# Kernel tuning notes

Hardware: AMD Instinct MI355X
Metric: run time of the kernel (lower is better)

## Reference

```python
import jax, jax.numpy as jnp
import numpy as np

D_MODEL, D_STATE, D_CONV, EXPAND, DT_RANK = 2048, 16, 4, 2, 128
D_INNER = EXPAND * D_MODEL
BATCH, SEQLEN = 4, 2048


def setup_inputs() -> dict:
    key = jax.random.key(0)
    ks = jax.random.split(key, 10)
    s = lambda fan_in: 1.0 / np.sqrt(fan_in)
    hidden_states = jax.random.normal(ks[0], (BATCH, SEQLEN, D_MODEL), jnp.float32)
    W_in = jax.random.normal(ks[1], (2 * D_INNER, D_MODEL), jnp.float32) * s(D_MODEL)
    conv_w = jax.random.normal(ks[2], (D_INNER, D_CONV), jnp.float32) * s(D_CONV)
    conv_b = jax.random.normal(ks[3], (D_INNER,), jnp.float32) * 0.02
    W_x = jax.random.normal(ks[4], (DT_RANK + 2 * D_STATE, D_INNER), jnp.float32) * s(D_INNER)
    W_dt = jax.random.normal(ks[5], (D_INNER, DT_RANK), jnp.float32) * s(DT_RANK)
    # dt bias init so softplus(dt+bias) lands in a realistic small-dt range
    dt = jnp.exp(jax.random.uniform(ks[6], (D_INNER,)) * (np.log(0.1) - np.log(1e-3)) + np.log(1e-3))
    dt_bias = dt + jnp.log(-jnp.expm1(-dt))  # inverse softplus
    # A = -[1..d_state] per channel (standard S4D-real init)
    A_log = jnp.log(jnp.tile(jnp.arange(1, D_STATE + 1, dtype=jnp.float32), (D_INNER, 1)))
    D = jnp.ones((D_INNER,), jnp.float32)
    W_out = jax.random.normal(ks[7], (D_MODEL, D_INNER), jnp.float32) * s(D_INNER)
    return dict(hidden_states=hidden_states, W_in=W_in, conv_w=conv_w, conv_b=conv_b,
                W_x=W_x, W_dt=W_dt, dt_bias=dt_bias, A_log=A_log, D=D, W_out=W_out)


def _mamba_forward(hidden_states, W_in, conv_w, conv_b, W_x, W_dt, dt_bias, A_log, D, W_out):
    B_, L, _ = hidden_states.shape
    d_inner, d_state = A_log.shape
    dt_rank = W_dt.shape[1]

    # in_proj: (B,L,2*d_inner)
    xz = jnp.einsum('bld,ed->ble', hidden_states, W_in)
    x, z = jnp.split(xz, 2, axis=-1)              # each (B,L,d_inner)

    # depthwise causal conv1d over time
    x_bdl = jnp.transpose(x, (0, 2, 1))           # (B,d_inner,L)
    x_conv = jax.lax.conv_general_dilated(
        x_bdl, conv_w[:, None, :], window_strides=(1,),
        padding=[(conv_w.shape[-1] - 1, 0)],
        feature_group_count=d_inner,
        dimension_numbers=('NCH', 'OIH', 'NCH'))
    x_conv = x_conv + conv_b[None, :, None]
    xact = jax.nn.silu(jnp.transpose(x_conv, (0, 2, 1)))   # (B,L,d_inner)

    # x_proj -> dt, B, C
    x_dbl = jnp.einsum('bld,ed->ble', xact, W_x)
    dt_lr, Bm, Cm = jnp.split(x_dbl, [dt_rank, dt_rank + d_state], axis=-1)
    dt = jnp.einsum('blr,dr->bld', dt_lr, W_dt)            # (B,L,d_inner)
    delta = jax.nn.softplus(dt + dt_bias)                   # (B,L,d_inner)

    A = -jnp.exp(A_log)                                     # (d_inner,d_state)

    # selective scan over time (time-major xs)
    def step(h, inp):
        u_t, dlt_t, b_t, c_t = inp                          # (B,d),(B,d),(B,n),(B,n)
        dA = jnp.exp(dlt_t[..., None] * A)                  # (B,d,n)
        h = h * dA + (dlt_t * u_t)[..., None] * b_t[:, None, :]
        y_t = jnp.einsum('bdn,bn->bd', h, c_t)
        return h, y_t

    xs = (jnp.transpose(xact, (1, 0, 2)),
          jnp.transpose(delta, (1, 0, 2)),
          jnp.transpose(Bm, (1, 0, 2)),
          jnp.transpose(Cm, (1, 0, 2)))
    h0 = jnp.zeros((B_, d_inner, d_state), xact.dtype)
    _, ys = jax.lax.scan(step, h0, xs)                      # ys: (L,B,d_inner)
    y = jnp.transpose(ys, (1, 0, 2)) + D * xact             # skip via D
    y = y * jax.nn.silu(z)                                  # gating

    return jnp.einsum('bld,od->blo', y, W_out)              # out_proj


def reference(hidden_states, W_in, conv_w, conv_b, W_x, W_dt, dt_bias, A_log, D, W_out):
    return _mamba_forward(hidden_states, W_in, conv_w, conv_b, W_x, W_dt,
                          dt_bias, A_log, D, W_out)
```

## Files before the change

kernel.cpp:

```cpp
#include <hip/hip_runtime.h>
#include <hip/hip_bf16.h>
#include <math.h>

#define D_MODEL 2048
#define D_STATE 16
#define D_CONV  4
#define DT_RANK 128
#define D_INNER 4096
#define BATCH   4
#define SEQLEN  2048
#define BL      (BATCH * SEQLEN)

#define NCHUNK 4
#define CHUNK  (SEQLEN / NCHUNK)
#define SCH    32
#define NTILE  (CHUNK / SCH)

typedef __hip_bfloat16 bf16;
typedef __attribute__((ext_vector_type(8))) short  short8;
typedef __attribute__((ext_vector_type(4))) float  f32x4;

__device__ __forceinline__ float bf2f(bf16 v) { return __bfloat162float(v); }
__device__ __forceinline__ bf16  f2bf(float v) { return __float2bfloat16(v); }
__device__ __forceinline__ float us2f(unsigned short v) {
    return __uint_as_float((unsigned)v << 16);
}
__device__ __forceinline__ void st1(float* p, float v) { *p = v; }
__device__ __forceinline__ void st1(bf16* p, float v)  { *p = f2bf(v); }
__device__ __forceinline__ float fast_rcp(float x) { return __builtin_amdgcn_rcpf(x); }

__device__ __forceinline__ void async_cp16(const void* g, void* l) {
    __builtin_amdgcn_global_load_lds(
        (const __attribute__((address_space(1))) void*)g,
        (__attribute__((address_space(3))) void*)l, 16, 0, 0);
}

template <int EPI, typename TC>
__global__ __launch_bounds__(256) void gemm_mfma_nt(
    const bf16* __restrict__ A, const bf16* __restrict__ B,
    TC* __restrict__ C, int M, int N, int K, int lda, int ldb, int ldc,
    const float* __restrict__ bias, bf16* __restrict__ aux,
    float* __restrict__ aux2)
{
    __shared__ bf16 As[128][64];
    __shared__ bf16 Bs[128][64];

    const int tid  = threadIdx.x;
    const int lane = tid & 63;
    const int wave = tid >> 6;
    const int wm   = (wave >> 1) * 64;
    const int wn   = (wave & 1) * 64;

    const int m0 = blockIdx.x * 128;
    const int n0 = blockIdx.y * 128;

    f32x4 acc[4][4] = {};

    const int srow = lane >> 3;
    const int scol = (lane & 7) * 8;

    for (int k0 = 0; k0 < K; k0 += 64) {
        __syncthreads();
#pragma unroll
        for (int i = 0; i < 4; ++i) {
            int seg = wave * 4 + i;
            int row = seg * 8 + srow;
            async_cp16(A + (size_t)(m0 + row) * lda + k0 + scol, &As[seg * 8][0]);
            async_cp16(B + (size_t)(n0 + row) * ldb + k0 + scol, &Bs[seg * 8][0]);
        }
        __syncthreads();

#pragma unroll
        for (int kk = 0; kk < 64; kk += 32) {
            short8 a[4], b[4];
            const int fr = lane & 15;
            const int fk = kk + (lane >> 4) * 8;
#pragma unroll
            for (int i = 0; i < 4; ++i) {
                a[i] = *(const short8*)&As[wm + i * 16 + fr][fk];
                b[i] = *(const short8*)&Bs[wn + i * 16 + fr][fk];
            }
#pragma unroll
            for (int i = 0; i < 4; ++i)
#pragma unroll
                for (int j = 0; j < 4; ++j)
                    acc[i][j] = __builtin_amdgcn_mfma_f32_16x16x32_bf16(
                        a[i], b[j], acc[i][j], 0, 0, 0);
        }
    }

#pragma unroll
    for (int i = 0; i < 4; ++i) {
        int row = m0 + wm + i * 16 + (lane >> 4) * 4;
#pragma unroll
        for (int j = 0; j < 4; ++j) {
            int col = n0 + wn + j * 16 + (lane & 15);
#pragma unroll
            for (int r = 0; r < 4; ++r) {
                float v = acc[i][j][r];
                if (EPI == 0) {
                    st1(C + (size_t)(row + r) * ldc + col, v);
                } else if (EPI == 1) {
                    if (col < DT_RANK)
                        aux[(size_t)(row + r) * DT_RANK + col] = f2bf(v);
                    else if (col < DT_RANK + 2 * D_STATE)
                        aux2[(size_t)(row + r) * (2 * D_STATE) + (col - DT_RANK)] = v;
                } else {
                    float x  = v + bias[col];
                    float sp = fmaxf(x, 0.f) + __logf(1.f + __expf(-fabsf(x)));
                    ((bf16*)C)[(size_t)(row + r) * ldc + col] = f2bf(sp);
                }
            }
        }
    }
}

__global__ void cvt_f32_bf16(const float* __restrict__ src,
                             bf16* __restrict__ dst, int n)
{
    int i = (blockIdx.x * blockDim.x + threadIdx.x) * 4;
    if (i >= n) return;
    float4 v = *(const float4*)(src + i);
    bf16 o[4] = { f2bf(v.x), f2bf(v.y), f2bf(v.z), f2bf(v.w) };
    *(ushort4*)(dst + i) = *(ushort4*)o;
}

__global__ void cvt_pad_wx(const float* __restrict__ src, bf16* __restrict__ dst)
{
    int i = (blockIdx.x * blockDim.x + threadIdx.x) * 4;
    if (i >= 256 * D_INNER) return;
    int row = i / D_INNER;
    bf16 o[4] = {};
    if (row < DT_RANK + 2 * D_STATE) {
        float4 v = *(const float4*)(src + i);
        o[0] = f2bf(v.x); o[1] = f2bf(v.y); o[2] = f2bf(v.z); o[3] = f2bf(v.w);
    }
    *(ushort4*)(dst + i) = *(ushort4*)o;
}

__global__ void conv_silu(const bf16* __restrict__ X,
                          const float* __restrict__ conv_w,
                          const float* __restrict__ conv_b,
                          bf16* __restrict__ xact)
{
    unsigned idx = blockIdx.x * blockDim.x + threadIdx.x;
    if (idx >= (unsigned)BL * D_INNER) return;
    int c = idx & (D_INNER - 1);
    unsigned bl = idx >> 12;
    int l = bl & (SEQLEN - 1);
    int b = bl >> 11;

    float acc = conv_b[c];
#pragma unroll
    for (int t = 0; t < D_CONV; ++t) {
        int ll = l - (D_CONV - 1) + t;
        if (ll >= 0)
            acc = fmaf(bf2f(X[((size_t)b * SEQLEN + ll) * D_INNER + c]),
                       conv_w[c * D_CONV + t], acc);
    }
    xact[(size_t)bl * D_INNER + c] = f2bf(acc * fast_rcp(1.f + __expf(-acc)));
}

__global__ __launch_bounds__(256, 8) void scan_part1(
    const bf16* __restrict__ U,
    const bf16* __restrict__ DLT,
    const float* __restrict__ BC,
    const float* __restrict__ A_log,
    float2* __restrict__ Hscr,
    float*  __restrict__ Sscr)
{
    __shared__ unsigned short Us[2][SCH][32];
    __shared__ unsigned short Ds[2][SCH][32];
    __shared__ float          Bs[2][SCH][16];

    const int b    = blockIdx.y;
    const int c    = blockIdx.z;
    const int d0   = blockIdx.x * 32;
    const int lane = threadIdx.x & 63;
    const int wave = threadIdx.x >> 6;
    const int sub  = lane & 7;
    const int grp  = lane >> 3;
    const int ci   = wave * 8 + grp;
    const int d    = d0 + ci;

    const float2 al = *(const float2*)&A_log[(size_t)d * D_STATE + 2 * sub];
    const float A0 = -__expf(al.x), A1 = -__expf(al.y);

    const size_t base = (size_t)b * SEQLEN + (size_t)c * CHUNK;

    const int r16 = lane >> 2;
    const int c8  = (lane & 3) * 8;
    const int c4f = (lane & 3) * 4;

    auto stage = [&](int bb, int l0) {
        if (wave == 0) {
#pragma unroll
            for (int i = 0; i < 2; ++i) {
                int row = i * 16 + r16;
                async_cp16(U + (base + l0 + row) * (size_t)D_INNER + d0 + c8,
                           &Us[bb][i * 16][0]);
            }
        } else if (wave == 1) {
#pragma unroll
            for (int i = 0; i < 2; ++i) {
                int row = i * 16 + r16;
                async_cp16(DLT + (base + l0 + row) * (size_t)D_INNER + d0 + c8,
                           &Ds[bb][i * 16][0]);
            }
        } else if (wave == 2) {
#pragma unroll
            for (int i = 0; i < 2; ++i) {
                int row = i * 16 + r16;
                async_cp16(BC + (base + l0 + row) * (2 * D_STATE) + c4f,
                           &Bs[bb][i * 16][0]);
            }
        }
    };

    float h0 = 0.f, h1 = 0.f, sdl = 0.f;

    stage(0, 0);
    __syncthreads();

    for (int t = 0; t < NTILE; ++t) {
        const int cur = t & 1, nxt = cur ^ 1;
        if (t + 1 < NTILE) stage(nxt, (t + 1) * SCH);

        for (int l = 0; l < SCH; ++l) {
            float u  = us2f(Us[cur][l][ci]);
            float dl = us2f(Ds[cur][l][ci]);
            float e0 = __expf(dl * A0);
            float e1 = __expf(dl * A1);
            float du = dl * u;
            float2 Bv = *(const float2*)&Bs[cur][l][2 * sub];
            h0 = fmaf(h0, e0, du * Bv.x);
            h1 = fmaf(h1, e1, du * Bv.y);
            sdl += dl;
        }
        __syncthreads();
    }

    const size_t idx = (size_t)(c * BATCH + b) * D_INNER + d;
    Hscr[idx * 8 + sub] = make_float2(h0, h1);
    if (sub == 0) Sscr[idx] = sdl;
}

__global__ void scan_combine(float2* __restrict__ Hscr,
                             const float* __restrict__ Sscr,
                             const float* __restrict__ A_log)
{
    int tid = blockIdx.x * blockDim.x + threadIdx.x;
    if (tid >= BATCH * D_INNER * 8) return;
    const int sub = tid & 7;
    const int d   = (tid >> 3) & (D_INNER - 1);
    const int b   = tid >> 15;

    const float2 al = *(const float2*)&A_log[(size_t)d * D_STATE + 2 * sub];
    const float A0 = -__expf(al.x), A1 = -__expf(al.y);

    float H0 = 0.f, H1 = 0.f;
#pragma unroll
    for (int c = 0; c < NCHUNK - 1; ++c) {
        const size_t idx = (size_t)(c * BATCH + b) * D_INNER + d;
        float2 hl = Hscr[idx * 8 + sub];
        float  s  = Sscr[idx];
        H0 = fmaf(H0, __expf(A0 * s), hl.x);
        H1 = fmaf(H1, __expf(A1 * s), hl.y);
        Hscr[idx * 8 + sub] = make_float2(H0, H1);
    }
}

__global__ __launch_bounds__(256, 8) void scan_main(
    const bf16* __restrict__ U,
    const bf16* __restrict__ DLT,
    const bf16* __restrict__ Z,
    const float* __restrict__ BC,
    const float* __restrict__ A_log,
    const float* __restrict__ Dp,
    const float2* __restrict__ Hscr,
    bf16* __restrict__ Y)
{
    __shared__ unsigned short Us[2][SCH][32];
    __shared__ unsigned short Ds[2][SCH][32];
    __shared__ unsigned short Zs[2][SCH][32];
    __shared__ float         BCs[2][SCH][32];

    const int b    = blockIdx.y;
    const int c    = blockIdx.z;
    const int d0   = blockIdx.x * 32;
    const int lane = threadIdx.x & 63;
    const int wave = threadIdx.x >> 6;
    const int sub  = lane & 7;
    const int grp  = lane >> 3;
    const int ci   = wave * 8 + grp;
    const int d    = d0 + ci;

    const float2 al = *(const float2*)&A_log[(size_t)d * D_STATE + 2 * sub];
    const float A0 = -__expf(al.x), A1 = -__expf(al.y);
    const float Dv = Dp[d];

    const size_t base = (size_t)b * SEQLEN + (size_t)c * CHUNK;

    const int r16 = lane >> 2;
    const int c8  = (lane & 3) * 8;
    const int r8  = lane >> 3;
    const int c4  = (lane & 7) * 4;

    auto stage = [&](int bb, int l0) {
        if (wave == 0) {
#pragma unroll
            for (int i = 0; i < 2; ++i) {
                int row = i * 16 + r16;
                async_cp16(U + (base + l0 + row) * (size_t)D_INNER + d0 + c8,
                           &Us[bb][i * 16][0]);
            }
        } else if (wave == 1) {
#pragma unroll
            for (int i = 0; i < 2; ++i) {
                int row = i * 16 + r16;
                async_cp16(DLT + (base + l0 + row) * (size_t)D_INNER + d0 + c8,
                           &Ds[bb][i * 16][0]);
            }
        } else if (wave == 2) {
#pragma unroll
            for (int i = 0; i < 2; ++i) {
                int row = i * 16 + r16;
                async_cp16(Z + (base + l0 + row) * (size_t)D_INNER + d0 + c8,
                           &Zs[bb][i * 16][0]);
            }
        } else {
#pragma unroll
            for (int i = 0; i < 4; ++i) {
                int row = i * 8 + r8;
                async_cp16(BC + (base + l0 + row) * (2 * D_STATE) + c4,
                           &BCs[bb][i * 8][0]);
            }
        }
    };

    float h0 = 0.f, h1 = 0.f;
    if (c > 0) {
        float2 hi = Hscr[((size_t)((c - 1) * BATCH + b) * D_INNER + d) * 8 + sub];
        h0 = hi.x; h1 = hi.y;
    }

    stage(0, 0);
    __syncthreads();

    for (int t = 0; t < NTILE; ++t) {
        const int cur = t & 1, nxt = cur ^ 1;
        if (t + 1 < NTILE) stage(nxt, (t + 1) * SCH);

        for (int l = 0; l < SCH; ++l) {
            float u  = us2f(Us[cur][l][ci]);
            float dl = us2f(Ds[cur][l][ci]);
            float e0 = __expf(dl * A0);
            float e1 = __expf(dl * A1);
            float du = dl * u;
            float2 Bv = *(const float2*)&BCs[cur][l][2 * sub];
            float2 Cv = *(const float2*)&BCs[cur][l][D_STATE + 2 * sub];
            h0 = fmaf(h0, e0, du * Bv.x);
            h1 = fmaf(h1, e1, du * Bv.y);
            float p = fmaf(h1, Cv.y, h0 * Cv.x);
            p += __shfl_xor(p, 1, 8);
            p += __shfl_xor(p, 2, 8);
            p += __shfl_xor(p, 4, 8);
            if (sub == 0) {
                float z = us2f(Zs[cur][l][ci]);
                float g = z * fast_rcp(1.f + __expf(-z));
                Y[(base + t * SCH + l) * (size_t)D_INNER + d] =
                    f2bf((p + Dv * u) * g);
            }
        }
        __syncthreads();
    }
}

extern "C" void kernel_launch(void* const* d_in, const int* in_sizes, int n_in,
                              void* d_out, int out_size, void* d_ws, size_t ws_size,
                              hipStream_t stream)
{
    const float* hs      = (const float*)d_in[0];
    const float* W_in    = (const float*)d_in[1];
    const float* conv_w  = (const float*)d_in[2];
    const float* conv_b  = (const float*)d_in[3];
    const float* W_x     = (const float*)d_in[4];
    const float* W_dt    = (const float*)d_in[5];
    const float* dt_bias = (const float*)d_in[6];
    const float* A_log   = (const float*)d_in[7];
    const float* Dp      = (const float*)d_in[8];
    const float* W_out   = (const float*)d_in[9];
    float* out = (float*)d_out;

    const size_t nBig = (size_t)BL * D_INNER;
    const size_t need = 2 * nBig * sizeof(bf16)
                      + (size_t)BL * 160 * sizeof(float);
    if (ws_size < need) {
        hipMemsetAsync(d_out, 0, (size_t)out_size * sizeof(float), stream);
        return;
    }

    bf16*  buf1  = (bf16*)d_ws;
    bf16*  buf2  = buf1 + nBig;
    float* BCbuf = (float*)(buf2 + nBig);
    bf16*  dtlr  = (bf16*)(BCbuf + (size_t)BL * 2 * D_STATE);
    bf16*  wxp   = dtlr + (size_t)BL * DT_RANK;
    bf16*  wdtb  = wxp;

    float2* Hscr = (float2*)dtlr;
    float*  Sscr = (float*)(Hscr + (size_t)(NCHUNK - 1) * BATCH * D_INNER * 8);

    const int nHS = BL * D_MODEL;
    const int nWI = 2 * D_INNER * D_MODEL;
    const int nWH = D_INNER * D_MODEL;
    bf16* hsb  = (bf16*)d_out;
    bf16* wb   = hsb + nHS;
    bf16* xact = (bf16*)d_out;

    cvt_f32_bf16<<<nHS / 1024, 256, 0, stream>>>(hs, hsb, nHS);
    cvt_f32_bf16<<<nWI / 1024, 256, 0, stream>>>(W_in, wb, nWI);
    gemm_mfma_nt<0, bf16><<<dim3(BL / 128, D_INNER / 128), 256, 0, stream>>>(
        hsb, wb + (size_t)nWH, buf2, BL, D_INNER, D_MODEL,
        D_MODEL, D_MODEL, D_INNER, nullptr, nullptr, nullptr);
    gemm_mfma_nt<0, bf16><<<dim3(BL / 128, D_INNER / 128), 256, 0, stream>>>(
        hsb, wb, buf1, BL, D_INNER, D_MODEL,
        D_MODEL, D_MODEL, D_INNER, nullptr, nullptr, nullptr);

    conv_silu<<<(BL * D_INNER + 255) / 256, 256, 0, stream>>>(
        buf1, conv_w, conv_b, xact);

    cvt_pad_wx<<<(256 * D_INNER) / 1024, 256, 0, stream>>>(W_x, wxp);
    gemm_mfma_nt<1, float><<<dim3(BL / 128, 2), 256, 0, stream>>>(
        xact, wxp, (float*)nullptr, BL, 256, D_INNER,
        D_INNER, D_INNER, 0, nullptr, dtlr, BCbuf);

    cvt_f32_bf16<<<(D_INNER * DT_RANK) / 1024, 256, 0, stream>>>(W_dt, wdtb,
                                                                 D_INNER * DT_RANK);
    gemm_mfma_nt<2, bf16><<<dim3(BL / 128, D_INNER / 128), 256, 0, stream>>>(
        dtlr, wdtb, buf1, BL, D_INNER, DT_RANK,
        DT_RANK, DT_RANK, D_INNER, dt_bias, nullptr, nullptr);

    scan_part1<<<dim3(D_INNER / 32, BATCH, NCHUNK - 1), 256, 0, stream>>>(
        xact, buf1, BCbuf, A_log, Hscr, Sscr);
    scan_combine<<<(BATCH * D_INNER * 8) / 256, 256, 0, stream>>>(
        Hscr, Sscr, A_log);
    scan_main<<<dim3(D_INNER / 32, BATCH, NCHUNK), 256, 0, stream>>>(
        xact, buf1, buf2, BCbuf, A_log, Dp, Hscr, buf2);

    cvt_f32_bf16<<<nWH / 1024, 256, 0, stream>>>(W_out, buf1, nWH);
    gemm_mfma_nt<0, float><<<dim3(BL / 128, D_MODEL / 128), 256, 0, stream>>>(
        buf2, buf1, out, BL, D_MODEL, D_INNER,
        D_INNER, D_INNER, D_MODEL, nullptr, nullptr, nullptr);
}
```

Baseline: 1.402 ms.

## Give scan threads four states each, read B/C from global, vectorize conv

```diff
diff --git a/kernel.cpp b/kernel.cpp
--- a/kernel.cpp
+++ b/kernel.cpp
@@ -33,6 +33,15 @@
     __builtin_amdgcn_global_load_lds(
         (const __attribute__((address_space(1))) void*)g,
         (__attribute__((address_space(3))) void*)l, 16, 0, 0);
+}
+
+__device__ __forceinline__ float quad_sum(float p) {
+    int q;
+    q = __builtin_amdgcn_update_dpp(0, __float_as_int(p), 0xB1, 0xF, 0xF, false);
+    p += __int_as_float(q);
+    q = __builtin_amdgcn_update_dpp(0, __float_as_int(p), 0x4E, 0xF, 0xF, false);
+    p += __int_as_float(q);
+    return p;
 }
 
 template <int EPI, typename TC>
@@ -144,80 +153,85 @@
                           bf16* __restrict__ xact)
 {
     unsigned idx = blockIdx.x * blockDim.x + threadIdx.x;
-    if (idx >= (unsigned)BL * D_INNER) return;
-    int c = idx & (D_INNER - 1);
-    unsigned bl = idx >> 12;
+    if (idx >= (unsigned)BL * (D_INNER / 8)) return;
+    int c8 = (idx & (D_INNER / 8 - 1)) * 8;
+    unsigned bl = idx >> 9;
     int l = bl & (SEQLEN - 1);
     int b = bl >> 11;
 
-    float acc = conv_b[c];
+    float acc[8];
+    float4 wv[8];
+#pragma unroll
+    for (int j = 0; j < 8; ++j) {
+        acc[j] = conv_b[c8 + j];
+        wv[j]  = *(const float4*)(conv_w + (c8 + j) * 4);
+    }
 #pragma unroll
     for (int t = 0; t < D_CONV; ++t) {
         int ll = l - (D_CONV - 1) + t;
-        if (ll >= 0)
-            acc = fmaf(bf2f(X[((size_t)b * SEQLEN + ll) * D_INNER + c]),
-                       conv_w[c * D_CONV + t], acc);
-    }
-    xact[(size_t)bl * D_INNER + c] = f2bf(acc * fast_rcp(1.f + __expf(-acc)));
-}
-
-__global__ __launch_bounds__(256, 8) void scan_part1(
+        if (ll >= 0) {
+            short8 xv = *(const short8*)(X + ((size_t)b * SEQLEN + ll) * D_INNER + c8);
+#pragma unroll
+            for (int j = 0; j < 8; ++j)
+                acc[j] = fmaf(us2f((unsigned short)xv[j]), (&wv[j].x)[t], acc[j]);
+        }
+    }
+    bf16 o[8];
+#pragma unroll
+    for (int j = 0; j < 8; ++j)
+        o[j] = f2bf(acc[j] * fast_rcp(1.f + __expf(-acc[j])));
+    *(short8*)(xact + (size_t)bl * D_INNER + c8) = *(short8*)o;
+}
+
+__global__ __launch_bounds__(256, 4) void scan_part1(
     const bf16* __restrict__ U,
     const bf16* __restrict__ DLT,
     const float* __restrict__ BC,
     const float* __restrict__ A_log,
-    float2* __restrict__ Hscr,
+    float4* __restrict__ Hscr,
     float*  __restrict__ Sscr)
 {
-    __shared__ unsigned short Us[2][SCH][32];
-    __shared__ unsigned short Ds[2][SCH][32];
-    __shared__ float          Bs[2][SCH][16];
+    __shared__ unsigned short Us[2][SCH][64];
+    __shared__ unsigned short Ds[2][SCH][64];
 
     const int b    = blockIdx.y;
     const int c    = blockIdx.z;
-    const int d0   = blockIdx.x * 32;
+    const int d0   = blockIdx.x * 64;
     const int lane = threadIdx.x & 63;
     const int wave = threadIdx.x >> 6;
-    const int sub  = lane & 7;
-    const int grp  = lane >> 3;
-    const int ci   = wave * 8 + grp;
+    const int sub  = lane & 3;
+    const int grp  = lane >> 2;
+    const int ci   = wave * 16 + grp;
     const int d    = d0 + ci;
 
-    const float2 al = *(const float2*)&A_log[(size_t)d * D_STATE + 2 * sub];
-    const float A0 = -__expf(al.x), A1 = -__expf(al.y);
+    const float4 al = *(const float4*)&A_log[(size_t)d * D_STATE + 4 * sub];
+    const float A0 = -__expf(al.x), A1 = -__expf(al.y),
+                A2 = -__expf(al.z), A3 = -__expf(al.w);
 
     const size_t base = (size_t)b * SEQLEN + (size_t)c * CHUNK;
 
-    const int r16 = lane >> 2;
-    const int c8  = (lane & 3) * 8;
-    const int c4f = (lane & 3) * 4;
+    const int sr = lane >> 3;
+    const int sc = (lane & 7) * 8;
 
     auto stage = [&](int bb, int l0) {
         if (wave == 0) {
 #pragma unroll
-            for (int i = 0; i < 2; ++i) {
-                int row = i * 16 + r16;
-                async_cp16(U + (base + l0 + row) * (size_t)D_INNER + d0 + c8,
-                           &Us[bb][i * 16][0]);
+            for (int i = 0; i < 4; ++i) {
+                int row = i * 8 + sr;
+                async_cp16(U + (base + l0 + row) * (size_t)D_INNER + d0 + sc,
+                           &Us[bb][i * 8][0]);
             }
         } else if (wave == 1) {
 #pragma unroll
-            for (int i = 0; i < 2; ++i) {
-                int row = i * 16 + r16;
-                async_cp16(DLT + (base + l0 + row) * (size_t)D_INNER + d0 + c8,
-                           &Ds[bb][i * 16][0]);
-            }
-        } else if (wave == 2) {
-#pragma unroll
-            for (int i = 0; i < 2; ++i) {
-                int row = i * 16 + r16;
-                async_cp16(BC + (base + l0 + row) * (2 * D_STATE) + c4f,
-                           &Bs[bb][i * 16][0]);
+            for (int i = 0; i < 4; ++i) {
+                int row = i * 8 + sr;
+                async_cp16(DLT + (base + l0 + row) * (size_t)D_INNER + d0 + sc,
+                           &Ds[bb][i * 8][0]);
             }
         }
     };
 
-    float h0 = 0.f, h1 = 0.f, sdl = 0.f;
+    float h0 = 0.f, h1 = 0.f, h2 = 0.f, h3 = 0.f, sdl = 0.f;
 
     stage(0, 0);
     __syncthreads();
@@ -226,122 +240,118 @@
         const int cur = t & 1, nxt = cur ^ 1;
         if (t + 1 < NTILE) stage(nxt, (t + 1) * SCH);
 
+#pragma unroll 8
         for (int l = 0; l < SCH; ++l) {
             float u  = us2f(Us[cur][l][ci]);
             float dl = us2f(Ds[cur][l][ci]);
-            float e0 = __expf(dl * A0);
-            float e1 = __expf(dl * A1);
+            float4 Bv = *(const float4*)(BC + (base + t * SCH + l) * (2 * D_STATE)
+                                         + 4 * sub);
             float du = dl * u;
-            float2 Bv = *(const float2*)&Bs[cur][l][2 * sub];
-            h0 = fmaf(h0, e0, du * Bv.x);
-            h1 = fmaf(h1, e1, du * Bv.y);
+            h0 = fmaf(h0, __expf(dl * A0), du * Bv.x);
+            h1 = fmaf(h1, __expf(dl * A1), du * Bv.y);
+            h2 = fmaf(h2, __expf(dl * A2), du * Bv.z);
+            h3 = fmaf(h3, __expf(dl * A3), du * Bv.w);
             sdl += dl;
         }
         __syncthreads();
     }
 
     const size_t idx = (size_t)(c * BATCH + b) * D_INNER + d;
-    Hscr[idx * 8 + sub] = make_float2(h0, h1);
+    Hscr[idx * 4 + sub] = make_float4(h0, h1, h2, h3);
     if (sub == 0) Sscr[idx] = sdl;
 }
 
-__global__ void scan_combine(float2* __restrict__ Hscr,
+__global__ void scan_combine(float4* __restrict__ Hscr,
                              const float* __restrict__ Sscr,
                              const float* __restrict__ A_log)
 {
     int tid = blockIdx.x * blockDim.x + threadIdx.x;
-    if (tid >= BATCH * D_INNER * 8) return;
-    const int sub = tid & 7;
-    const int d   = (tid >> 3) & (D_INNER - 1);
-    const int b   = tid >> 15;
-
-    const float2 al = *(const float2*)&A_log[(size_t)d * D_STATE + 2 * sub];
-    const float A0 = -__expf(al.x), A1 = -__expf(al.y);
-
-    float H0 = 0.f, H1 = 0.f;
+    if (tid >= BATCH * D_INNER * 4) return;
+    const int sub = tid & 3;
+    const int d   = (tid >> 2) & (D_INNER - 1);
+    const int b   = tid >> 14;
+
+    const float4 al = *(const float4*)&A_log[(size_t)d * D_STATE + 4 * sub];
+    const float A0 = -__expf(al.x), A1 = -__expf(al.y),
+                A2 = -__expf(al.z), A3 = -__expf(al.w);
+
+    float H0 = 0.f, H1 = 0.f, H2 = 0.f, H3 = 0.f;
 #pragma unroll
     for (int c = 0; c < NCHUNK - 1; ++c) {
         const size_t idx = (size_t)(c * BATCH + b) * D_INNER + d;
-        float2 hl = Hscr[idx * 8 + sub];
+        float4 hl = Hscr[idx * 4 + sub];
         float  s  = Sscr[idx];
         H0 = fmaf(H0, __expf(A0 * s), hl.x);
         H1 = fmaf(H1, __expf(A1 * s), hl.y);
-        Hscr[idx * 8 + sub] = make_float2(H0, H1);
-    }
-}
-
-__global__ __launch_bounds__(256, 8) void scan_main(
+        H2 = fmaf(H2, __expf(A2 * s), hl.z);
+        H3 = fmaf(H3, __expf(A3 * s), hl.w);
+        Hscr[idx * 4 + sub] = make_float4(H0, H1, H2, H3);
+    }
+}
+
+__global__ __launch_bounds__(256, 4) void scan_main(
     const bf16* __restrict__ U,
     const bf16* __restrict__ DLT,
     const bf16* __restrict__ Z,
     const float* __restrict__ BC,
     const float* __restrict__ A_log,
     const float* __restrict__ Dp,
-    const float2* __restrict__ Hscr,
+    const float4* __restrict__ Hscr,
     bf16* __restrict__ Y)
 {
-    __shared__ unsigned short Us[2][SCH][32];
-    __shared__ unsigned short Ds[2][SCH][32];
-    __shared__ unsigned short Zs[2][SCH][32];
-    __shared__ float         BCs[2][SCH][32];
+    __shared__ unsigned short Us[2][SCH][64];
+    __shared__ unsigned short Ds[2][SCH][64];
+    __shared__ unsigned short Zs[2][SCH][64];
 
     const int b    = blockIdx.y;
     const int c    = blockIdx.z;
-    const int d0   = blockIdx.x * 32;
+    const int d0   = blockIdx.x * 64;
     const int lane = threadIdx.x & 63;
     const int wave = threadIdx.x >> 6;
-    const int sub  = lane & 7;
-    const int grp  = lane >> 3;
-    const int ci   = wave * 8 + grp;
+    const int sub  = lane & 3;
+    const int grp  = lane >> 2;
+    const int ci   = wave * 16 + grp;
     const int d    = d0 + ci;
 
-    const float2 al = *(const float2*)&A_log[(size_t)d * D_STATE + 2 * sub];
-    const float A0 = -__expf(al.x), A1 = -__expf(al.y);
+    const float4 al = *(const float4*)&A_log[(size_t)d * D_STATE + 4 * sub];
+    const float A0 = -__expf(al.x), A1 = -__expf(al.y),
+                A2 = -__expf(al.z), A3 = -__expf(al.w);
     const float Dv = Dp[d];
 
     const size_t base = (size_t)b * SEQLEN + (size_t)c * CHUNK;
 
-    const int r16 = lane >> 2;
-    const int c8  = (lane & 3) * 8;
-    const int r8  = lane >> 3;
-    const int c4  = (lane & 7) * 4;
+    const int sr = lane >> 3;
+    const int sc = (lane & 7) * 8;
 
     auto stage = [&](int bb, int l0) {
         if (wave == 0) {
 #pragma unroll
-            for (int i = 0; i < 2; ++i) {
-                int row = i * 16 + r16;
-                async_cp16(U + (base + l0 + row) * (size_t)D_INNER + d0 + c8,
-                           &Us[bb][i * 16][0]);
+            for (int i = 0; i < 4; ++i) {
+                int row = i * 8 + sr;
+                async_cp16(U + (base + l0 + row) * (size_t)D_INNER + d0 + sc,
+                           &Us[bb][i * 8][0]);
             }
         } else if (wave == 1) {
 #pragma unroll
-            for (int i = 0; i < 2; ++i) {
-                int row = i * 16 + r16;
-                async_cp16(DLT + (base + l0 + row) * (size_t)D_INNER + d0 + c8,
-                           &Ds[bb][i * 16][0]);
+            for (int i = 0; i < 4; ++i) {
+                int row = i * 8 + sr;
+                async_cp16(DLT + (base + l0 + row) * (size_t)D_INNER + d0 + sc,
+                           &Ds[bb][i * 8][0]);
             }
         } else if (wave == 2) {
 #pragma unroll
-            for (int i = 0; i < 2; ++i) {
-                int row = i * 16 + r16;
-                async_cp16(Z + (base + l0 + row) * (size_t)D_INNER + d0 + c8,
-                           &Zs[bb][i * 16][0]);
-            }
-        } else {
-#pragma unroll
-            for (int i = 0; i < 4; ++i) {
-                int row = i * 8 + r8;
-                async_cp16(BC + (base + l0 + row) * (2 * D_STATE) + c4,
-                           &BCs[bb][i * 8][0]);
+            for (int i = 0; i < 4; ++i) {
+                int row = i * 8 + sr;
+                async_cp16(Z + (base + l0 + row) * (size_t)D_INNER + d0 + sc,
+                           &Zs[bb][i * 8][0]);
             }
         }
     };
 
-    float h0 = 0.f, h1 = 0.f;
+    float h0 = 0.f, h1 = 0.f, h2 = 0.f, h3 = 0.f;
     if (c > 0) {
-        float2 hi = Hscr[((size_t)((c - 1) * BATCH + b) * D_INNER + d) * 8 + sub];
-        h0 = hi.x; h1 = hi.y;
+        float4 hi = Hscr[((size_t)((c - 1) * BATCH + b) * D_INNER + d) * 4 + sub];
+        h0 = hi.x; h1 = hi.y; h2 = hi.z; h3 = hi.w;
     }
 
     stage(0, 0);
@@ -351,20 +361,20 @@
         const int cur = t & 1, nxt = cur ^ 1;
         if (t + 1 < NTILE) stage(nxt, (t + 1) * SCH);
 
+#pragma unroll 8
         for (int l = 0; l < SCH; ++l) {
             float u  = us2f(Us[cur][l][ci]);
             float dl = us2f(Ds[cur][l][ci]);
-            float e0 = __expf(dl * A0);
-            float e1 = __expf(dl * A1);
+            const float* bcp = BC + (base + t * SCH + l) * (2 * D_STATE);
+            float4 Bv = *(const float4*)(bcp + 4 * sub);
+            float4 Cv = *(const float4*)(bcp + D_STATE + 4 * sub);
             float du = dl * u;
-            float2 Bv = *(const float2*)&BCs[cur][l][2 * sub];
-            float2 Cv = *(const float2*)&BCs[cur][l][D_STATE + 2 * sub];
-            h0 = fmaf(h0, e0, du * Bv.x);
-            h1 = fmaf(h1, e1, du * Bv.y);
-            float p = fmaf(h1, Cv.y, h0 * Cv.x);
-            p += __shfl_xor(p, 1, 8);
-            p += __shfl_xor(p, 2, 8);
-            p += __shfl_xor(p, 4, 8);
+            h0 = fmaf(h0, __expf(dl * A0), du * Bv.x);
+            h1 = fmaf(h1, __expf(dl * A1), du * Bv.y);
+            h2 = fmaf(h2, __expf(dl * A2), du * Bv.z);
+            h3 = fmaf(h3, __expf(dl * A3), du * Bv.w);
+            float p = fmaf(h3, Cv.w, fmaf(h2, Cv.z, fmaf(h1, Cv.y, h0 * Cv.x)));
+            p = quad_sum(p);
             if (sub == 0) {
                 float z = us2f(Zs[cur][l][ci]);
                 float g = z * fast_rcp(1.f + __expf(-z));
@@ -407,8 +417,8 @@
     bf16*  wxp   = dtlr + (size_t)BL * DT_RANK;
     bf16*  wdtb  = wxp;
 
-    float2* Hscr = (float2*)dtlr;
-    float*  Sscr = (float*)(Hscr + (size_t)(NCHUNK - 1) * BATCH * D_INNER * 8);
+    float4* Hscr = (float4*)dtlr;
+    float*  Sscr = (float*)(Hscr + (size_t)(NCHUNK - 1) * BATCH * D_INNER * 4);
 
     const int nHS = BL * D_MODEL;
     const int nWI = 2 * D_INNER * D_MODEL;
@@ -426,7 +436,7 @@
         hsb, wb, buf1, BL, D_INNER, D_MODEL,
         D_MODEL, D_MODEL, D_INNER, nullptr, nullptr, nullptr);
 
-    conv_silu<<<(BL * D_INNER + 255) / 256, 256, 0, stream>>>(
+    conv_silu<<<(BL * (D_INNER / 8)) / 256, 256, 0, stream>>>(
         buf1, conv_w, conv_b, xact);
 
     cvt_pad_wx<<<(256 * D_INNER) / 1024, 256, 0, stream>>>(W_x, wxp);
@@ -440,11 +450,11 @@
         dtlr, wdtb, buf1, BL, D_INNER, DT_RANK,
         DT_RANK, DT_RANK, D_INNER, dt_bias, nullptr, nullptr);
 
-    scan_part1<<<dim3(D_INNER / 32, BATCH, NCHUNK - 1), 256, 0, stream>>>(
+    scan_part1<<<dim3(D_INNER / 64, BATCH, NCHUNK - 1), 256, 0, stream>>>(
         xact, buf1, BCbuf, A_log, Hscr, Sscr);
-    scan_combine<<<(BATCH * D_INNER * 8) / 256, 256, 0, stream>>>(
+    scan_combine<<<(BATCH * D_INNER * 4) / 256, 256, 0, stream>>>(
         Hscr, Sscr, A_log);
-    scan_main<<<dim3(D_INNER / 32, BATCH, NCHUNK), 256, 0, stream>>>(
+    scan_main<<<dim3(D_INNER / 64, BATCH, NCHUNK), 256, 0, stream>>>(
         xact, buf1, buf2, BCbuf, A_log, Dp, Hscr, buf2);
 
     cvt_f32_bf16<<<nWH / 1024, 256, 0, stream>>>(W_out, buf1, nWH);
```

Measured after the change: 1.351 ms. 3.6% less time.
